# Performance work log

Measured on AMD Instinct MI355X. Metric: run time of the kernel, lower is better.

## Reference

```python
import jax, jax.numpy as jnp
import numpy as np

LATENT = 32
GRID = 32
G1 = GRID + 1  # 33 samples per axis (align_corners grid)
HID = 128
N_POINTS = 1048576


def _trilinear_sample(emb, points):
    """Faithful F.grid_sample(mode='bilinear', padding_mode='zeros', align_corners=True).
    emb: [(G1)^3, C] flat table; points: [n,3] in [-1,1], (x,y,z) -> (W,H,D)."""
    C = emb.shape[1]
    # torch .view(1, C, D, H, W) on the flat [(G1)^3 * C] buffer: same reshape here.
    vol = emb.reshape(C, G1, G1, G1).transpose(1, 2, 3, 0)  # [D, H, W, C]
    # align_corners=True: u in [-1,1] -> pixel coord (u+1)/2 * (size-1)
    coords = (points + 1.0) * (0.5 * (G1 - 1))
    x, y, z = coords[:, 0], coords[:, 1], coords[:, 2]
    x0 = jnp.floor(x); y0 = jnp.floor(y); z0 = jnp.floor(z)
    fx = x - x0; fy = y - y0; fz = z - z0
    x0i = x0.astype(jnp.int32); y0i = y0.astype(jnp.int32); z0i = z0.astype(jnp.int32)
    x1i = x0i + 1; y1i = y0i + 1; z1i = z0i + 1

    def corner(zi, yi, xi, w):
        valid = ((zi >= 0) & (zi < G1) & (yi >= 0) & (yi < G1)
                 & (xi >= 0) & (xi < G1))
        zc = jnp.clip(zi, 0, G1 - 1)
        yc = jnp.clip(yi, 0, G1 - 1)
        xc = jnp.clip(xi, 0, G1 - 1)
        v = vol[zc, yc, xc]  # [n, C] gather
        return v * (w * valid.astype(w.dtype))[:, None]

    wx0, wx1 = 1.0 - fx, fx
    wy0, wy1 = 1.0 - fy, fy
    wz0, wz1 = 1.0 - fz, fz
    lat = (corner(z0i, y0i, x0i, wz0 * wy0 * wx0)
           + corner(z0i, y0i, x1i, wz0 * wy0 * wx1)
           + corner(z0i, y1i, x0i, wz0 * wy1 * wx0)
           + corner(z0i, y1i, x1i, wz0 * wy1 * wx1)
           + corner(z1i, y0i, x0i, wz1 * wy0 * wx0)
           + corner(z1i, y0i, x1i, wz1 * wy0 * wx1)
           + corner(z1i, y1i, x0i, wz1 * wy1 * wx0)
           + corner(z1i, y1i, x1i, wz1 * wy1 * wx1))
    return lat  # [n, C]


def setup_inputs() -> dict:
    key = jax.random.key(0)
    ks = jax.random.split(key, 8)
    points = jax.random.uniform(ks[0], (N_POINTS, 3), dtype=jnp.float32)  # in [0,1) subset of [-1,1]
    emb = jax.random.normal(ks[1], (G1 ** 3, LATENT), dtype=jnp.float32)
    w1 = jax.random.normal(ks[2], (LATENT, HID), dtype=jnp.float32) * 0.05
    b1 = jax.random.normal(ks[3], (HID,), dtype=jnp.float32) * 0.05
    w2 = jax.random.normal(ks[4], (HID, HID), dtype=jnp.float32) * 0.05
    b2 = jax.random.normal(ks[5], (HID,), dtype=jnp.float32) * 0.05
    w3 = jax.random.normal(ks[6], (HID, 1), dtype=jnp.float32) * 0.05
    b3 = jax.random.normal(ks[7], (1,), dtype=jnp.float32) * 0.05
    return {"points": points, "emb": emb, "w1": w1, "b1": b1,
            "w2": w2, "b2": b2, "w3": w3, "b3": b3}


def reference(points, emb, w1, b1, w2, b2, w3, b3):
    lat = _trilinear_sample(emb, points)                # [n, latent]
    h = jax.nn.relu(lat @ w1 + b1)                      # [n, hid]
    h = jax.nn.relu(h @ w2 + b2)                        # [n, hid]
    sdf = jnp.tanh(h @ w3 + b3)                         # [n, 1]
    return sdf
```

## Files before the change

kernel.cpp:

```cpp
#include <hip/hip_runtime.h>
#include <hip/hip_bf16.h>

#define NPTS 1048576
#define G1I  33
#define NV   35937
#define NC   32
#define HIDD 128

typedef _Float16 h8 __attribute__((ext_vector_type(8)));
typedef _Float16 h4 __attribute__((ext_vector_type(4)));
typedef float    f4 __attribute__((ext_vector_type(4)));

#define WS_A1  0
#define WS_A2  8192
#define WS_EMB 65536
#define WS_NEED (WS_EMB + NV*NC*2)


__global__ __launch_bounds__(256) void vox_prep(
    const float* __restrict__ emb, const float* __restrict__ w1,
    const float* __restrict__ w2, char* __restrict__ ws)
{
    __shared__ _Float16 tile[256][NC];
    const int b = blockIdx.x, t = threadIdx.x;
    _Float16* embh = (_Float16*)(ws + WS_EMB);
    if (b < 141) {
        const int v = b*256 + t;
        #pragma unroll
        for (int c = 0; c < NC; ++c) {
            float val = (v < NV) ? emb[c*NV + v] : 0.f;
            tile[t][c] = (_Float16)val;
        }
        __syncthreads();
        if (v < NV) {
            uint4* dst = (uint4*)(embh + v*NC);
            const uint4* src = (const uint4*)&tile[t][0];
            #pragma unroll
            for (int j = 0; j < 4; ++j) dst[j] = src[j];
        }
    } else if (t < 64) {
        const int l = t, colh = l & 15, gq = l >> 4;
        _Float16* a1f = (_Float16*)(ws + WS_A1);
        _Float16* a2f = (_Float16*)(ws + WS_A2);
        #pragma unroll
        for (int t8 = 0; t8 < 8; ++t8) {
            h8 fr;
            #pragma unroll
            for (int i = 0; i < 8; ++i) {
                int k = 16*(i>>2) + 4*gq + (i&3);
                fr[i] = (_Float16)w1[k*HIDD + 16*t8 + colh];
            }
            *(h8*)(a1f + (t8*64 + l)*8) = fr;
        }
        for (int t2 = 0; t2 < 8; ++t2)
            for (int ks = 0; ks < 4; ++ks) {
                h8 fr;
                for (int i = 0; i < 8; ++i) {
                    int k = 32*ks + 16*(i>>2) + 4*gq + (i&3);
                    fr[i] = (_Float16)w2[k*HIDD + 16*t2 + colh];
                }
                *(h8*)(a2f + ((t2*4+ks)*64 + l)*8) = fr;
            }
    }
}

__global__ __launch_bounds__(256, 2) void vox_main(
    const float* __restrict__ points, const char* __restrict__ ws,
    const float* __restrict__ b1, const float* __restrict__ b2,
    const float* __restrict__ w3, const float* __restrict__ b3v,
    float* __restrict__ out)
{
    __shared__ _Float16 latl[256][40];
    __shared__ uint4    a2l[2048];

    const int tid  = threadIdx.x;
    const int lane = tid & 63;
    const int wv   = tid >> 6;
    const int gq   = lane >> 4;
    const int colh = lane & 15;

    const uint4* a2g = (const uint4*)(ws + WS_A2);
    #pragma unroll
    for (int j = 0; j < 8; ++j) a2l[j*256 + tid] = a2g[j*256 + tid];

    const _Float16* embh = (const _Float16*)(ws + WS_EMB);
    const int p = blockIdx.x*256 + tid;
    const float px = points[3*p+0], py = points[3*p+1], pz = points[3*p+2];
    const float xc = (px + 1.f)*16.f, yc = (py + 1.f)*16.f, zc = (pz + 1.f)*16.f;
    const float xf = floorf(xc), yf = floorf(yc), zf = floorf(zc);
    const float fx = xc - xf, fy = yc - yf, fz = zc - zf;
    const int x0 = (int)xf, y0 = (int)yf, z0 = (int)zf;
    const float wzv[2] = {1.f-fz, fz}, wyv[2] = {1.f-fy, fy}, wxv[2] = {1.f-fx, fx};

    h8 acc8[4];
    #pragma unroll
    for (int j = 0; j < 4; ++j) acc8[j] = (h8){0,0,0,0,0,0,0,0};
    #pragma unroll
    for (int cz = 0; cz < 2; ++cz)
    #pragma unroll
    for (int cy = 0; cy < 2; ++cy) {
        const int vb = ((z0+cz)*G1I + (y0+cy))*G1I + x0;
        const float wzy = wzv[cz]*wyv[cy];
        #pragma unroll
        for (int cx = 0; cx < 2; ++cx) {
            const _Float16 wh = (_Float16)(wzy * wxv[cx]);
            const h8 wp = {wh,wh,wh,wh,wh,wh,wh,wh};
            const h8* rowp = (const h8*)(embh + (vb + cx)*NC);
            #pragma unroll
            for (int j = 0; j < 4; ++j) acc8[j] += wp * rowp[j];
        }
    }
    {
        uint4* lr = (uint4*)&latl[tid][0];
        #pragma unroll
        for (int j = 0; j < 4; ++j) lr[j] = *(uint4*)&acc8[j];
    }
    __syncthreads();

    const h8* a1g = (const h8*)(ws + WS_A1);
    h8 a1fr[8];
    #pragma unroll
    for (int t8 = 0; t8 < 8; ++t8) a1fr[t8] = a1g[t8*64 + lane];
    f4 b1v[8];
    #pragma unroll
    for (int t8 = 0; t8 < 8; ++t8) b1v[t8] = *(const f4*)(b1 + 16*t8 + 4*gq);

    h8 B2f[4][4];
    #pragma unroll
    for (int pt = 0; pt < 4; ++pt) {
        const int row = wv*64 + pt*16 + colh;
        const h4 blo = *(const h4*)&latl[row][4*gq];
        const h4 bhi = *(const h4*)&latl[row][16 + 4*gq];
        h8 bf;
        #pragma unroll
        for (int j = 0; j < 4; ++j) { bf[j] = blo[j]; bf[4+j] = bhi[j]; }
        f4 acc1[8];
        #pragma unroll
        for (int t8 = 0; t8 < 8; ++t8) acc1[t8] = b1v[t8];
        #pragma unroll
        for (int t8 = 0; t8 < 8; ++t8)
            acc1[t8] = __builtin_amdgcn_mfma_f32_16x16x32_f16(a1fr[t8], bf, acc1[t8], 0, 0, 0);
        #pragma unroll
        for (int ks = 0; ks < 4; ++ks) {
            h8 bb;
            #pragma unroll
            for (int r = 0; r < 4; ++r) {
                bb[r]   = (_Float16)fmaxf(acc1[2*ks  ][r], 0.f);
                bb[4+r] = (_Float16)fmaxf(acc1[2*ks+1][r], 0.f);
            }
            B2f[pt][ks] = bb;
        }
    }

    float part[4] = {0.f, 0.f, 0.f, 0.f};
    #pragma unroll
    for (int t2 = 0; t2 < 8; ++t2) {
        const f4 b2q = *(const f4*)(b2 + 16*t2 + 4*gq);
        const f4 w3q = *(const f4*)(w3 + 16*t2 + 4*gq);
        f4 acc2[4];
        #pragma unroll
        for (int pt = 0; pt < 4; ++pt) acc2[pt] = b2q;
        #pragma unroll
        for (int ks = 0; ks < 4; ++ks) {
            const h8 a2fr = *(const h8*)&a2l[(t2*4 + ks)*64 + lane];
            #pragma unroll
            for (int pt = 0; pt < 4; ++pt)
                acc2[pt] = __builtin_amdgcn_mfma_f32_16x16x32_f16(a2fr, B2f[pt][ks], acc2[pt], 0, 0, 0);
        }
        #pragma unroll
        for (int pt = 0; pt < 4; ++pt)
            #pragma unroll
            for (int r = 0; r < 4; ++r)
                part[pt] += fmaxf(acc2[pt][r], 0.f) * w3q[r];
    }

    float sv = 0.f;
    #pragma unroll
    for (int pt = 0; pt < 4; ++pt) {
        float s = part[pt];
        s += __shfl_xor(s, 16);
        s += __shfl_xor(s, 32);
        if (gq == pt) sv = s;
    }
    const float zi = sv + b3v[0];
    const float e  = __expf(2.f*zi);
    out[blockIdx.x*256 + tid] = (e - 1.f) / (e + 1.f);
}

extern "C" void kernel_launch(void* const* d_in, const int* in_sizes, int n_in,
                              void* d_out, int out_size, void* d_ws, size_t ws_size,
                              hipStream_t stream)
{
    const float* points = (const float*)d_in[0];
    const float* emb    = (const float*)d_in[1];
    const float* w1     = (const float*)d_in[2];
    const float* b1     = (const float*)d_in[3];
    const float* w2     = (const float*)d_in[4];
    const float* b2     = (const float*)d_in[5];
    const float* w3     = (const float*)d_in[6];
    const float* b3     = (const float*)d_in[7];
    float* out = (float*)d_out;
    char*  ws  = (char*)d_ws;
    if (ws_size < (size_t)WS_NEED) return;

    hipLaunchKernelGGL(vox_prep, dim3(142), dim3(256), 0, stream, emb, w1, w2, ws);
    hipLaunchKernelGGL(vox_main, dim3(NPTS/256), dim3(256), 0, stream,
                       points, ws, b1, b2, w3, b3, out);
}
```

Measured before the change: 155.3 us.

## Parallelize weight prep across blocks, read W2 fragments from global, pack ReLU converts

The weight-fragment prep that ran on a single wavefront is now spread over nine blocks: eight handle W2 and one handles W1. The main kernel no longer stages the 32 KB W2 fragment table into LDS per block and instead reads the fragments directly from global memory, relying on L1/L2 caching. This cuts LDS use and the staging loads, which may raise occupancy. The ReLU-and-convert to fp16 now uses packed round-toward-zero conversion with a packed max, which slightly changes rounding relative to round-to-nearest.

```diff
diff --git a/kernel.cpp b/kernel.cpp
--- a/kernel.cpp
+++ b/kernel.cpp
@@ -7,9 +7,10 @@
 #define NC   32
 #define HIDD 128
 
-typedef _Float16 h8 __attribute__((ext_vector_type(8)));
-typedef _Float16 h4 __attribute__((ext_vector_type(4)));
-typedef float    f4 __attribute__((ext_vector_type(4)));
+typedef _Float16 h8  __attribute__((ext_vector_type(8)));
+typedef _Float16 h4  __attribute__((ext_vector_type(4)));
+typedef __fp16   p2  __attribute__((ext_vector_type(2)));
+typedef float    f4  __attribute__((ext_vector_type(4)));
 
 #define WS_A1  0
 #define WS_A2  8192
@@ -38,29 +39,33 @@
             #pragma unroll
             for (int j = 0; j < 4; ++j) dst[j] = src[j];
         }
-    } else if (t < 64) {
-        const int l = t, colh = l & 15, gq = l >> 4;
+    } else if (b < 149) {
+        const int t2 = b - 141;
+        const int ks = t >> 6, l = t & 63;
+        const int gq = l >> 4, colh = l & 15;
+        _Float16* a2f = (_Float16*)(ws + WS_A2);
+        h8 fr;
+        #pragma unroll
+        for (int i = 0; i < 8; ++i) {
+            const int k = 32*ks + 16*(i>>2) + 4*gq + (i&3);
+            fr[i] = (_Float16)w2[k*HIDD + 16*t2 + colh];
+        }
+        *(h8*)(a2f + ((t2*4+ks)*64 + l)*8) = fr;
+    } else {
         _Float16* a1f = (_Float16*)(ws + WS_A1);
-        _Float16* a2f = (_Float16*)(ws + WS_A2);
-        #pragma unroll
-        for (int t8 = 0; t8 < 8; ++t8) {
+        #pragma unroll
+        for (int it = 0; it < 2; ++it) {
+            const int item = t + it*256;
+            const int t8 = item >> 6, l = item & 63;
+            const int gq = l >> 4, colh = l & 15;
             h8 fr;
             #pragma unroll
             for (int i = 0; i < 8; ++i) {
-                int k = 16*(i>>2) + 4*gq + (i&3);
+                const int k = 16*(i>>2) + 4*gq + (i&3);
                 fr[i] = (_Float16)w1[k*HIDD + 16*t8 + colh];
             }
             *(h8*)(a1f + (t8*64 + l)*8) = fr;
         }
-        for (int t2 = 0; t2 < 8; ++t2)
-            for (int ks = 0; ks < 4; ++ks) {
-                h8 fr;
-                for (int i = 0; i < 8; ++i) {
-                    int k = 32*ks + 16*(i>>2) + 4*gq + (i&3);
-                    fr[i] = (_Float16)w2[k*HIDD + 16*t2 + colh];
-                }
-                *(h8*)(a2f + ((t2*4+ks)*64 + l)*8) = fr;
-            }
     }
 }
 
@@ -71,17 +76,12 @@
     float* __restrict__ out)
 {
     __shared__ _Float16 latl[256][40];
-    __shared__ uint4    a2l[2048];
 
     const int tid  = threadIdx.x;
     const int lane = tid & 63;
     const int wv   = tid >> 6;
     const int gq   = lane >> 4;
     const int colh = lane & 15;
-
-    const uint4* a2g = (const uint4*)(ws + WS_A2);
-    #pragma unroll
-    for (int j = 0; j < 8; ++j) a2l[j*256 + tid] = a2g[j*256 + tid];
 
     const _Float16* embh = (const _Float16*)(ws + WS_EMB);
     const int p = blockIdx.x*256 + tid;
@@ -142,16 +142,17 @@
             acc1[t8] = __builtin_amdgcn_mfma_f32_16x16x32_f16(a1fr[t8], bf, acc1[t8], 0, 0, 0);
         #pragma unroll
         for (int ks = 0; ks < 4; ++ks) {
-            h8 bb;
-            #pragma unroll
-            for (int r = 0; r < 4; ++r) {
-                bb[r]   = (_Float16)fmaxf(acc1[2*ks  ][r], 0.f);
-                bb[4+r] = (_Float16)fmaxf(acc1[2*ks+1][r], 0.f);
-            }
-            B2f[pt][ks] = bb;
-        }
-    }
-
+            union { h8 v; p2 h[4]; } u;
+            const p2 z = {(__fp16)0, (__fp16)0};
+            u.h[0] = __builtin_elementwise_max(__builtin_amdgcn_cvt_pkrtz(acc1[2*ks  ][0], acc1[2*ks  ][1]), z);
+            u.h[1] = __builtin_elementwise_max(__builtin_amdgcn_cvt_pkrtz(acc1[2*ks  ][2], acc1[2*ks  ][3]), z);
+            u.h[2] = __builtin_elementwise_max(__builtin_amdgcn_cvt_pkrtz(acc1[2*ks+1][0], acc1[2*ks+1][1]), z);
+            u.h[3] = __builtin_elementwise_max(__builtin_amdgcn_cvt_pkrtz(acc1[2*ks+1][2], acc1[2*ks+1][3]), z);
+            B2f[pt][ks] = u.v;
+        }
+    }
+
+    const h8* a2g = (const h8*)(ws + WS_A2);
     float part[4] = {0.f, 0.f, 0.f, 0.f};
     #pragma unroll
     for (int t2 = 0; t2 < 8; ++t2) {
@@ -162,7 +163,7 @@
         for (int pt = 0; pt < 4; ++pt) acc2[pt] = b2q;
         #pragma unroll
         for (int ks = 0; ks < 4; ++ks) {
-            const h8 a2fr = *(const h8*)&a2l[(t2*4 + ks)*64 + lane];
+            const h8 a2fr = a2g[(t2*4 + ks)*64 + lane];
             #pragma unroll
             for (int pt = 0; pt < 4; ++pt)
                 acc2[pt] = __builtin_amdgcn_mfma_f32_16x16x32_f16(a2fr, B2f[pt][ks], acc2[pt], 0, 0, 0);
@@ -203,7 +204,7 @@
     char*  ws  = (char*)d_ws;
     if (ws_size < (size_t)WS_NEED) return;
 
-    hipLaunchKernelGGL(vox_prep, dim3(142), dim3(256), 0, stream, emb, w1, w2, ws);
+    hipLaunchKernelGGL(vox_prep, dim3(150), dim3(256), 0, stream, emb, w1, w2, ws);
     hipLaunchKernelGGL(vox_main, dim3(NPTS/256), dim3(256), 0, stream,
                        points, ws, b1, b2, w3, b3, out);
 }
```

Measured after the change: 161.5 us. +4.0%, slower.
